# Optimization experiments

Measured on AMD Instinct MI355X. Metric: run time of the kernel, lower is better.

The kernel has to match this reference:

```python
import jax, jax.numpy as jnp
import numpy as np

SEQ, BATCH = 2048, 32
ENC_HS, DEC_HS = 512, 1024

def setup_inputs() -> dict:
    key = jax.random.key(0)
    k1, k2, k3, k4, k5 = jax.random.split(key, 5)
    return {
        "hidden": jax.random.normal(k1, (BATCH, DEC_HS), dtype=jnp.float32),
        "encoder_outputs": jax.random.normal(k2, (SEQ, BATCH, 2 * ENC_HS), dtype=jnp.float32),
        "attn_w": jax.random.normal(k3, (2 * ENC_HS + DEC_HS, DEC_HS), dtype=jnp.float32) * 0.02,
        "attn_b": jax.random.normal(k4, (DEC_HS,), dtype=jnp.float32) * 0.02,
        "v": jax.random.normal(k5, (DEC_HS,), dtype=jnp.float32),
    }

def reference(hidden, encoder_outputs, attn_w, attn_b, v):
    # encoder_outputs: [S, B, 2*enc_hs] -> [B, S, 2*enc_hs]
    enc = jnp.transpose(encoder_outputs, (1, 0, 2))
    B, S, _ = enc.shape
    # hidden: [B, dec_hs] broadcast to [B, S, dec_hs]
    h = jnp.broadcast_to(hidden[:, None, :], (B, S, hidden.shape[-1]))
    cat = jnp.concatenate([h, enc], axis=2)            # [B, S, 2*enc_hs+dec_hs]
    energy = jnp.tanh(cat @ attn_w + attn_b)            # [B, S, dec_hs]
    scores = jnp.einsum("bsd,d->bs", energy, v)        # [B, S]
    return jax.nn.softmax(scores, axis=1)
```

## Files before the change

### kernel.cpp

```cpp
#include <hip/hip_runtime.h>


typedef _Float16 f16;
typedef _Float16 half4 __attribute__((ext_vector_type(4)));
typedef _Float16 half8 __attribute__((ext_vector_type(8)));
typedef float f32x4 __attribute__((ext_vector_type(4)));

#define KDIM 1024
#define SEQ  2048
#define MROWS 65536

typedef __attribute__((address_space(1))) void gvoid;
typedef __attribute__((address_space(3))) void svoid;

__device__ __forceinline__ void gload_lds16(const void* g, void* l) {
    __builtin_amdgcn_global_load_lds((const gvoid*)g, (svoid*)l, 16, 0, 0);
}

__global__ __launch_bounds__(256) void prep_w(const float* __restrict__ w,
                                              f16* __restrict__ wt) {
    int idx  = blockIdx.x * 256 + threadIdx.x;
    int kblk = idx & 3;
    int nloc = (idx >> 2) & 127;
    int tk   = idx >> 9;
    int ks   = tk & 31, nq = tk >> 5;
    int n_g  = nq * 128 + nloc;
    int kb   = 1024 + ks * 32 + kblk * 8;
    half8 h;
#pragma unroll
    for (int j = 0; j < 8; ++j)
        h[j] = (f16)w[(size_t)(kb + j) * 1024 + n_g];
    int p = nloc * 4 + ((kblk + (nloc >> 1)) & 3);
    *(half8*)&wt[(size_t)tk * 4096 + p * 8] = h;
}

__global__ __launch_bounds__(256) void prep_hb(const float* __restrict__ hidden,
                                               const float* __restrict__ attn_w,
                                               const float* __restrict__ attn_b,
                                               float* __restrict__ hb) {
    int b = blockIdx.x >> 2;
    int n = (blockIdx.x & 3) * 256 + threadIdx.x;
    const float* h = hidden + (size_t)b * 1024;
    float acc = attn_b[n];
#pragma unroll 8
    for (int k = 0; k < 1024; ++k)
        acc += h[k] * attn_w[(size_t)k * 1024 + n];
    hb[(size_t)b * 1024 + n] = acc;
}

__global__ __launch_bounds__(256, 3)
void fused_energy(const float* __restrict__ enc, const f16* __restrict__ wt,
                  const float* __restrict__ hb, const float* __restrict__ vvec,
                  float* __restrict__ partout) {
    __shared__ f16 Bls[2][4096];
    __shared__ f16 Als[4096];
    __shared__ float red[2][128];

    const int tid  = threadIdx.x;
    const int lane = tid & 63;
    const int wv   = tid >> 6;
    const int wm   = wv >> 1;
    const int wn   = wv & 1;
    const int l15  = lane & 15;
    const int l4   = lane >> 4;

    const int bid   = blockIdx.x;
    const int xcd   = bid & 7;
    const int chunk = bid >> 3;
    const int mt    = xcd * 64 + (chunk >> 3);
    const int nq    = chunk & 7;
    const int mrow0 = mt * 128;
    const int ncol0 = nq * 128;

    const char* wtNq = (const char*)wt + (size_t)nq * 32 * 8192;

    const int arow0 = tid >> 3;
    const int ak16  = tid & 7;
    const float* aG = enc + (size_t)(mrow0 + arow0) * KDIM + ak16 * 4;
    char* const aW  = (char*)Als + arow0 * 64 + ak16 * 8;

    int aOffB[4], bOffB[4];
#pragma unroll
    for (int mi = 0; mi < 4; ++mi) {
        int r = wm * 64 + mi * 16 + l15;
        aOffB[mi] = r * 64 + l4 * 16;
    }
#pragma unroll
    for (int nj = 0; nj < 4; ++nj) {
        int n = wn * 64 + nj * 16 + l15;
        bOffB[nj] = (n * 4 + ((l4 + (n >> 1)) & 3)) * 16;
    }

    const f32x4 zero = {0.f, 0.f, 0.f, 0.f};
    f32x4 acc[4][4];
#pragma unroll
    for (int mi = 0; mi < 4; ++mi)
#pragma unroll
        for (int nj = 0; nj < 4; ++nj) acc[mi][nj] = zero;

    f32x4 rA[4];
    half8 bf[4], af[4];

#define WAITV(N) asm volatile("s_waitcnt vmcnt(" #N ")" ::: "memory")
#define LGKM0    asm volatile("s_waitcnt lgkmcnt(0)" ::: "memory")
#define BAR      __builtin_amdgcn_s_barrier()

#define STAGE_B(KS)                                                           \
    {                                                                         \
        const char* s_ = wtNq + (size_t)(KS) * 8192 + tid * 16;               \
        char* d_ = (char*)&Bls[(KS) & 1][0] + tid * 16;                       \
        gload_lds16(s_, d_);                                                  \
        gload_lds16(s_ + 4096, d_ + 4096);                                    \
    }
#define LOADA(KS)                                                             \
    {                                                                         \
        const float* p_ = aG + (KS) * 32;                                     \
        rA[0] = *(const f32x4*)(p_);                                          \
        rA[1] = *(const f32x4*)(p_ + 32 * KDIM);                              \
        rA[2] = *(const f32x4*)(p_ + 64 * KDIM);                              \
        rA[3] = *(const f32x4*)(p_ + 96 * KDIM);                              \
    }
#define CVTA()                                                                \
    {                                                                         \
        _Pragma("unroll") for (int i = 0; i < 4; ++i) {                       \
            half4 h_;                                                         \
            _Pragma("unroll") for (int j = 0; j < 4; ++j)                     \
                h_[j] = (f16)rA[i][j];                                        \
            *(half4*)(aW + i * 2048) = h_;                                    \
        }                                                                     \
    }
#define COMPUTE(KS)                                                           \
    {                                                                         \
        const char* bb_ = (const char*)&Bls[(KS) & 1][0];                     \
        _Pragma("unroll") for (int nj = 0; nj < 4; ++nj)                      \
            bf[nj] = *(const half8*)(bb_ + bOffB[nj]);                        \
        _Pragma("unroll") for (int mi = 0; mi < 4; ++mi)                      \
            af[mi] = *(const half8*)((char*)Als + aOffB[mi]);                 \
        LGKM0;                                                                \
        __builtin_amdgcn_s_setprio(1);                                        \
        _Pragma("unroll") for (int mi = 0; mi < 4; ++mi)                      \
            _Pragma("unroll") for (int nj = 0; nj < 4; ++nj)                  \
                acc[mi][nj] = __builtin_amdgcn_mfma_f32_16x16x32_f16(         \
                    af[mi], bf[nj], acc[mi][nj], 0, 0, 0);                    \
        __builtin_amdgcn_s_setprio(0);                                        \
    }

    LOADA(0);
    STAGE_B(0);

    for (int ks = 0; ks < 31; ++ks) {
        LGKM0;
        BAR;
        WAITV(2);
        CVTA();
        LOADA(ks + 1);
        STAGE_B(ks + 1);
        WAITV(6);
        LGKM0;
        BAR;
        COMPUTE(ks);
    }
    LGKM0;
    BAR;
    WAITV(2);
    CVTA();
    WAITV(0);
    LGKM0;
    BAR;
    COMPUTE(31);

#undef STAGE_B
#undef LOADA
#undef CVTA
#undef COMPUTE

    float vv[4];
#pragma unroll
    for (int nj = 0; nj < 4; ++nj)
        vv[nj] = vvec[ncol0 + wn * 64 + nj * 16 + l15];
#pragma unroll
    for (int mi = 0; mi < 4; ++mi) {
#pragma unroll
        for (int rg = 0; rg < 4; ++rg) {
            int rl = wm * 64 + mi * 16 + l4 * 4 + rg;
            const float* hbrow = hb + (size_t)((mrow0 + rl) & 31) * 1024
                                 + ncol0 + wn * 64 + l15;
            float sum = 0.f;
#pragma unroll
            for (int nj = 0; nj < 4; ++nj) {
                float e  = acc[mi][nj][rg] + hbrow[nj * 16];
                float e2 = __expf(2.f * e);
                sum += (1.f - 2.f / (e2 + 1.f)) * vv[nj];
            }
            float p = sum;
            p += __shfl_xor(p, 1);
            p += __shfl_xor(p, 2);
            p += __shfl_xor(p, 4);
            p += __shfl_xor(p, 8);
            if (l15 == 0) red[wn][rl] = p;
        }
    }
    __syncthreads();
    if (tid < 128) {
        float s = red[0][tid] + red[1][tid];
        partout[(size_t)nq * MROWS + mrow0 + tid] = s;
    }
}

__global__ __launch_bounds__(256) void softmax_rows(const float* __restrict__ part,
                                                    float* __restrict__ out) {
    const int b = blockIdx.x;
    const int tid  = threadIdx.x;
    const int lane = tid & 63;
    const int wv   = tid >> 6;
    __shared__ float sred[4];
    __shared__ float ssum[4];
    float x[8];
    float mx = -3.4e38f;
#pragma unroll
    for (int j = 0; j < 8; ++j) {
        int flat = (tid + j * 256) * 32 + b;
        float v = 0.f;
#pragma unroll
        for (int q = 0; q < 8; ++q) v += part[(size_t)q * MROWS + flat];
        x[j] = v;
        mx = fmaxf(mx, v);
    }
#pragma unroll
    for (int o = 1; o < 64; o <<= 1) mx = fmaxf(mx, __shfl_xor(mx, o));
    if (lane == 0) sred[wv] = mx;
    __syncthreads();
    mx = fmaxf(fmaxf(sred[0], sred[1]), fmaxf(sred[2], sred[3]));
    float s = 0.f;
#pragma unroll
    for (int j = 0; j < 8; ++j) { x[j] = __expf(x[j] - mx); s += x[j]; }
#pragma unroll
    for (int o = 1; o < 64; o <<= 1) s += __shfl_xor(s, o);
    if (lane == 0) ssum[wv] = s;
    __syncthreads();
    s = ssum[0] + ssum[1] + ssum[2] + ssum[3];
    float inv = 1.f / s;
#pragma unroll
    for (int j = 0; j < 8; ++j) out[(size_t)b * SEQ + tid + j * 256] = x[j] * inv;
}

extern "C" void kernel_launch(void* const* d_in, const int* in_sizes, int n_in,
                              void* d_out, int out_size, void* d_ws, size_t ws_size,
                              hipStream_t stream) {
    const float* hidden = (const float*)d_in[0];
    const float* enc    = (const float*)d_in[1];
    const float* attn_w = (const float*)d_in[2];
    const float* attn_b = (const float*)d_in[3];
    const float* v      = (const float*)d_in[4];
    float* out = (float*)d_out;

    f16*   wt   = (f16*)d_ws;
    float* hb   = (float*)((char*)d_ws + 2097152);
    float* part = (float*)((char*)d_ws + 2097152 + 131072);

    prep_w<<<512, 256, 0, stream>>>(attn_w, wt);
    prep_hb<<<128, 256, 0, stream>>>(hidden, attn_w, attn_b, hb);
    fused_energy<<<4096, 256, 0, stream>>>(enc, wt, hb, v, part);
    softmax_rows<<<32, 256, 0, stream>>>(part, out);
}
```

Measured before the change: 290.4 us.

## Load B fragments straight into registers and double-buffer padded A in LDS

The weight operand is re-laid out so each lane's MFMA fragment is contiguous, and is loaded straight from global memory into registers instead of being staged through LDS. The A tile is double-buffered in LDS with a padded 80-byte row stride to avoid bank conflicts, and the loop is unrolled by two so loads for future steps overlap compute and need one barrier per step. This reduces LDS traffic and barriers but raises register pressure, so launch bounds drop from 3 to 2 blocks per CU, costing occupancy.

```diff
diff --git a/kernel.cpp b/kernel.cpp
--- a/kernel.cpp
+++ b/kernel.cpp
@@ -10,28 +10,20 @@
 #define SEQ  2048
 #define MROWS 65536
 
-typedef __attribute__((address_space(1))) void gvoid;
-typedef __attribute__((address_space(3))) void svoid;
-
-__device__ __forceinline__ void gload_lds16(const void* g, void* l) {
-    __builtin_amdgcn_global_load_lds((const gvoid*)g, (svoid*)l, 16, 0, 0);
-}
-
 __global__ __launch_bounds__(256) void prep_w(const float* __restrict__ w,
-                                              f16* __restrict__ wt) {
-    int idx  = blockIdx.x * 256 + threadIdx.x;
-    int kblk = idx & 3;
-    int nloc = (idx >> 2) & 127;
-    int tk   = idx >> 9;
-    int ks   = tk & 31, nq = tk >> 5;
-    int n_g  = nq * 128 + nloc;
-    int kb   = 1024 + ks * 32 + kblk * 8;
+                                              f16* __restrict__ wt2) {
+    int t  = blockIdx.x * 256 + threadIdx.x;
+    int l  = t & 63;
+    int gk = t >> 6;
+    int g  = gk & 63;
+    int ks = gk >> 6;
+    int kb = 1024 + ks * 32 + (l >> 4) * 8;
+    int n  = g * 16 + (l & 15);
     half8 h;
 #pragma unroll
     for (int j = 0; j < 8; ++j)
-        h[j] = (f16)w[(size_t)(kb + j) * 1024 + n_g];
-    int p = nloc * 4 + ((kblk + (nloc >> 1)) & 3);
-    *(half8*)&wt[(size_t)tk * 4096 + p * 8] = h;
+        h[j] = (f16)w[(size_t)(kb + j) * 1024 + n];
+    *(half8*)&wt2[(size_t)t * 8] = h;
 }
 
 __global__ __launch_bounds__(256) void prep_hb(const float* __restrict__ hidden,
@@ -48,12 +40,11 @@
     hb[(size_t)b * 1024 + n] = acc;
 }
 
-__global__ __launch_bounds__(256, 3)
-void fused_energy(const float* __restrict__ enc, const f16* __restrict__ wt,
+__global__ __launch_bounds__(256, 2)
+void fused_energy(const float* __restrict__ enc, const f16* __restrict__ wt2,
                   const float* __restrict__ hb, const float* __restrict__ vvec,
                   float* __restrict__ partout) {
-    __shared__ f16 Bls[2][4096];
-    __shared__ f16 Als[4096];
+    __shared__ __align__(16) char AB[2][10240];
     __shared__ float red[2][128];
 
     const int tid  = threadIdx.x;
@@ -66,29 +57,22 @@
 
     const int bid   = blockIdx.x;
     const int xcd   = bid & 7;
-    const int chunk = bid >> 3;
-    const int mt    = xcd * 64 + (chunk >> 3);
-    const int nq    = chunk & 7;
+    const int c     = bid >> 3;
+    const int mt    = xcd * 64 + (c >> 3);
+    const int nq    = c & 7;
     const int mrow0 = mt * 128;
     const int ncol0 = nq * 128;
 
-    const char* wtNq = (const char*)wt + (size_t)nq * 32 * 8192;
-
-    const int arow0 = tid >> 3;
-    const int ak16  = tid & 7;
-    const float* aG = enc + (size_t)(mrow0 + arow0) * KDIM + ak16 * 4;
-    char* const aW  = (char*)Als + arow0 * 64 + ak16 * 8;
-
-    int aOffB[4], bOffB[4];
+    const float* aSrc = enc + (size_t)(mrow0 + (tid >> 3)) * KDIM + (tid & 7) * 4;
+    const int awByte  = (tid >> 3) * 80 + (tid & 7) * 8;
+
+    const int gbase = nq * 8 + wn * 4;
+
+    int aOff[4];
 #pragma unroll
     for (int mi = 0; mi < 4; ++mi) {
         int r = wm * 64 + mi * 16 + l15;
-        aOffB[mi] = r * 64 + l4 * 16;
-    }
-#pragma unroll
-    for (int nj = 0; nj < 4; ++nj) {
-        int n = wn * 64 + nj * 16 + l15;
-        bOffB[nj] = (n * 4 + ((l4 + (n >> 1)) & 3)) * 16;
+        aOff[mi] = r * 80 + l4 * 16;
     }
 
     const f32x4 zero = {0.f, 0.f, 0.f, 0.f};
@@ -98,80 +82,64 @@
 #pragma unroll
         for (int nj = 0; nj < 4; ++nj) acc[mi][nj] = zero;
 
-    f32x4 rA[4];
-    half8 bf[4], af[4];
+    f32x4 rA0[4], rA1[4];
+    half8 bfE[4], bfO[4], af[4];
 
 #define WAITV(N) asm volatile("s_waitcnt vmcnt(" #N ")" ::: "memory")
 #define LGKM0    asm volatile("s_waitcnt lgkmcnt(0)" ::: "memory")
 #define BAR      __builtin_amdgcn_s_barrier()
 
-#define STAGE_B(KS)                                                           \
-    {                                                                         \
-        const char* s_ = wtNq + (size_t)(KS) * 8192 + tid * 16;               \
-        char* d_ = (char*)&Bls[(KS) & 1][0] + tid * 16;                       \
-        gload_lds16(s_, d_);                                                  \
-        gload_lds16(s_ + 4096, d_ + 4096);                                    \
-    }
-#define LOADA(KS)                                                             \
-    {                                                                         \
-        const float* p_ = aG + (KS) * 32;                                     \
-        rA[0] = *(const f32x4*)(p_);                                          \
-        rA[1] = *(const f32x4*)(p_ + 32 * KDIM);                              \
-        rA[2] = *(const f32x4*)(p_ + 64 * KDIM);                              \
-        rA[3] = *(const f32x4*)(p_ + 96 * KDIM);                              \
-    }
-#define CVTA()                                                                \
-    {                                                                         \
-        _Pragma("unroll") for (int i = 0; i < 4; ++i) {                       \
-            half4 h_;                                                         \
-            _Pragma("unroll") for (int j = 0; j < 4; ++j)                     \
-                h_[j] = (f16)rA[i][j];                                        \
-            *(half4*)(aW + i * 2048) = h_;                                    \
-        }                                                                     \
-    }
-#define COMPUTE(KS)                                                           \
-    {                                                                         \
-        const char* bb_ = (const char*)&Bls[(KS) & 1][0];                     \
-        _Pragma("unroll") for (int nj = 0; nj < 4; ++nj)                      \
-            bf[nj] = *(const half8*)(bb_ + bOffB[nj]);                        \
-        _Pragma("unroll") for (int mi = 0; mi < 4; ++mi)                      \
-            af[mi] = *(const half8*)((char*)Als + aOffB[mi]);                 \
-        LGKM0;                                                                \
-        __builtin_amdgcn_s_setprio(1);                                        \
-        _Pragma("unroll") for (int mi = 0; mi < 4; ++mi)                      \
-            _Pragma("unroll") for (int nj = 0; nj < 4; ++nj)                  \
-                acc[mi][nj] = __builtin_amdgcn_mfma_f32_16x16x32_f16(         \
-                    af[mi], bf[nj], acc[mi][nj], 0, 0, 0);                    \
-        __builtin_amdgcn_s_setprio(0);                                        \
-    }
-
-    LOADA(0);
-    STAGE_B(0);
-
-    for (int ks = 0; ks < 31; ++ks) {
-        LGKM0;
-        BAR;
-        WAITV(2);
-        CVTA();
-        LOADA(ks + 1);
-        STAGE_B(ks + 1);
-        WAITV(6);
-        LGKM0;
-        BAR;
-        COMPUTE(ks);
-    }
-    LGKM0;
-    BAR;
-    WAITV(2);
-    CVTA();
+#define LOADA(W, R)                                                           \
+    { _Pragma("unroll") for (int i = 0; i < 4; ++i)                           \
+        R[i] = *(const f32x4*)(aSrc + (size_t)(i * 32) * KDIM + (W) * 32); }
+#define LOADB(W, BF)                                                          \
+    { _Pragma("unroll") for (int nj = 0; nj < 4; ++nj)                        \
+        BF[nj] = *(const half8*)(wt2 +                                        \
+            ((size_t)((W) * 64 + gbase + nj) * 64 + lane) * 8); }
+#define CVWR(P, R)                                                            \
+    { char* b_ = AB[P];                                                       \
+      _Pragma("unroll") for (int i = 0; i < 4; ++i) {                         \
+          half4 h_;                                                           \
+          _Pragma("unroll") for (int j = 0; j < 4; ++j) h_[j] = (f16)R[i][j]; \
+          *(half4*)(b_ + awByte + i * 2560) = h_;                             \
+      } }
+#define COMPUTE(P, BF)                                                        \
+    { const char* s_ = AB[P];                                                 \
+      _Pragma("unroll") for (int j = 0; j < 4; ++j)                           \
+          af[j] = *(const half8*)(s_ + aOff[j]);                              \
+      __builtin_amdgcn_s_setprio(1);                                          \
+      _Pragma("unroll") for (int mi = 0; mi < 4; ++mi)                        \
+          _Pragma("unroll") for (int nj = 0; nj < 4; ++nj)                    \
+              acc[mi][nj] = __builtin_amdgcn_mfma_f32_16x16x32_f16(           \
+                  af[mi], BF[nj], acc[mi][nj], 0, 0, 0);                      \
+      __builtin_amdgcn_s_setprio(0); }
+
+    LOADA(0, rA0);
     WAITV(0);
-    LGKM0;
-    BAR;
-    COMPUTE(31);
-
-#undef STAGE_B
+    CVWR(0, rA0);
+    LOADA(1, rA1);
+    LOADB(0, bfE);
+
+    for (int t = 0; t < 30; t += 2) {
+        LOADA(t + 2, rA0); LOADB(t + 1, bfO);
+        WAITV(8); LGKM0; BAR;
+        CVWR(1, rA1);
+        COMPUTE(0, bfE);
+        LOADA(t + 3, rA1); LOADB(t + 2, bfE);
+        WAITV(8); LGKM0; BAR;
+        CVWR(0, rA0);
+        COMPUTE(1, bfO);
+    }
+    LOADB(31, bfO);
+    WAITV(4); LGKM0; BAR;
+    CVWR(1, rA1);
+    COMPUTE(0, bfE);
+    WAITV(0); LGKM0; BAR;
+    COMPUTE(1, bfO);
+
 #undef LOADA
-#undef CVTA
+#undef LOADB
+#undef CVWR
 #undef COMPUTE
 
     float vv[4];
@@ -254,12 +222,12 @@
     const float* v      = (const float*)d_in[4];
     float* out = (float*)d_out;
 
-    f16*   wt   = (f16*)d_ws;
+    f16*   wt2  = (f16*)d_ws;
     float* hb   = (float*)((char*)d_ws + 2097152);
     float* part = (float*)((char*)d_ws + 2097152 + 131072);
 
-    prep_w<<<512, 256, 0, stream>>>(attn_w, wt);
+    prep_w<<<512, 256, 0, stream>>>(attn_w, wt2);
     prep_hb<<<128, 256, 0, stream>>>(hidden, attn_w, attn_b, hb);
-    fused_energy<<<4096, 256, 0, stream>>>(enc, wt, hb, v, part);
+    fused_energy<<<4096, 256, 0, stream>>>(enc, wt2, hb, v, part);
     softmax_rows<<<32, 256, 0, stream>>>(part, out);
 }
```

New measurement: 273.6 us. 1.06x faster.
